# Optimization experiments

Measured on AMD Instinct MI355X. Metric: run time of the kernel, lower is better.

The kernel has to match this reference:

```python
import jax, jax.numpy as jnp
import numpy as np

LAMBDA = 25.0
MU = 25.0
NU = 1.0
ALPHA = 0.25
EPS = 1e-4
NUM_MATCHES = (20, 4)


def _cdist(a, b):
    # a: (B, Na, D), b: (B, Nb, D) -> euclidean distances (B, Na, Nb)
    d2 = (jnp.sum(a * a, axis=-1)[:, :, None]
          + jnp.sum(b * b, axis=-1)[:, None, :]
          - 2.0 * jnp.einsum('bnd,bmd->bnm', a, b))
    return jnp.sqrt(jnp.maximum(d2, 0.0))


def _nearest_neighbors(input_maps, candidate_maps, distances, num_matches):
    # Faithful to lightly.models.utils.nearest_neighbors:
    #  1) for each input element find its nearest candidate (argmin over last dim)
    #  2) keep the num_matches input elements with smallest nn distance
    # Indices are non-differentiable in torch, so stop_gradient on distances.
    distances = jax.lax.stop_gradient(distances)
    nn_idx = jnp.argmin(distances, axis=-1)           # (B, Na)
    nn_val = jnp.min(distances, axis=-1)              # (B, Na)
    _, min_idx = jax.lax.top_k(-nn_val, num_matches)  # smallest num_matches -> (B, M)
    filt_in = jnp.take_along_axis(input_maps, min_idx[..., None], axis=1)      # (B, M, C)
    cand_nn = jnp.take_along_axis(candidate_maps, nn_idx[..., None], axis=1)   # (B, Na, C)
    filt_cand = jnp.take_along_axis(cand_nn, min_idx[..., None], axis=1)       # (B, M, C)
    return filt_in, filt_cand


def _mse(a, b):
    return jnp.mean((a - b) ** 2)


def _variance_loss(x):
    # torch.var default is unbiased (ddof=1)
    std = jnp.sqrt(jnp.var(x, axis=0, ddof=1) + EPS)
    return jnp.mean(jax.nn.relu(1.0 - std))


def _covariance_loss(x):
    n, d = x.shape
    x = x - jnp.mean(x, axis=0)
    cov = (x.T @ x) / (n - 1)                         # (D, D)
    off = cov - jnp.diag(jnp.diag(cov))
    return jnp.sum(off ** 2) / d


def _global_loss(z_a, z_b):
    inv = _mse(z_a, z_b)
    var = 0.5 * (_variance_loss(z_a) + _variance_loss(z_b))
    cov = _covariance_loss(z_a) + _covariance_loss(z_b)
    return LAMBDA * inv + MU * var + NU * cov


def _local_loss(za, zb, ga, gb):
    B = za.shape[0]
    za = za.reshape(B, -1, za.shape[-1])              # (B, H*W, C)
    zb = zb.reshape(B, -1, zb.shape[-1])
    ga = ga.reshape(B, -1, 2)                          # (B, H*W, 2)
    gb = gb.reshape(B, -1, 2)
    has_local_view = za.shape[1] != zb.shape[1]
    nm = NUM_MATCHES[1] if has_local_view else NUM_MATCHES[0]
    # L2 feature-space matching
    fa, na = _nearest_neighbors(za, zb, _cdist(za, zb), nm)
    fb, nb = _nearest_neighbors(zb, za, _cdist(zb, za), nm)
    inv = 0.5 * _mse(fa, na) + 0.5 * _mse(fb, nb)
    # Grid (spatial) matching
    fa, na = _nearest_neighbors(za, zb, _cdist(ga, gb), NUM_MATCHES[0])
    fb, nb = _nearest_neighbors(zb, za, _cdist(gb, ga), NUM_MATCHES[1])
    inv = inv + 0.5 * _mse(fa, na) + 0.5 * _mse(fb, nb)
    return LAMBDA * inv


def setup_inputs() -> dict:
    key = jax.random.key(0)
    k1, k2, k3, k4, k5, k6 = jax.random.split(key, 6)
    B, D = 128, 8192
    H = W = 7
    return {
        'z_a': jax.random.normal(k1, (B, D), dtype=jnp.float32),
        'z_b': jax.random.normal(k2, (B, D), dtype=jnp.float32),
        'z_a_local_features': jax.random.normal(k3, (B, H, W, D), dtype=jnp.float32),
        'z_b_local_features': jax.random.normal(k4, (B, H, W, D), dtype=jnp.float32),
        'grid_a': jax.random.uniform(k5, (B, H, W, 2), dtype=jnp.float32),
        'grid_b': jax.random.uniform(k6, (B, H, W, 2), dtype=jnp.float32),
    }


def reference(z_a, z_b, z_a_local_features, z_b_local_features, grid_a, grid_b):
    g = _global_loss(z_a, z_b)
    l = _local_loss(z_a_local_features, z_b_local_features, grid_a, grid_b)
    return ALPHA * g + (1.0 - ALPHA) * l
```

## Files before the change

### kernel.cpp

```cpp
#include <hip/hip_runtime.h>
#include <math.h>

#define BATCH 128
#define DIM   8192
#define HW    49
#define PAIRS 2401
#define SLOT  2512

#define WS_MSE    0
#define WS_VARA   1
#define WS_VARB   2
#define WS_DIAGA  3
#define WS_DIAGB  4
#define WS_S1     5
#define WS_S2     6
#define WS_S3     7
#define WS_S4     8
#define WS_SK2A   9
#define WS_SK2B   10
#define COLS_OFF    16
#define GRAMA_OFF   32784
#define GRAMB_OFF   49168
#define GK2PART_OFF 65552
#define L1PART_BIG  2162704
#define WS_NEED_FLOATS (L1PART_BIG + 256 * SLOT)
#define L1PART_SMALL 65552

typedef __attribute__((ext_vector_type(8))) short bf16x8;
typedef __attribute__((ext_vector_type(4))) float f32x4;

__device__ __forceinline__ unsigned cvtpk(float lo, float hi) {
    unsigned r;
    asm("v_cvt_pk_bf16_f32 %0, %1, %2" : "=v"(r) : "v"(lo), "v"(hi));
    return r;
}
__device__ __forceinline__ bf16x8 cvt8(f32x4 a, f32x4 b) {
    union { unsigned u[4]; bf16x8 v; } r;
    r.u[0] = cvtpk(a.x, a.y); r.u[1] = cvtpk(a.z, a.w);
    r.u[2] = cvtpk(b.x, b.y); r.u[3] = cvtpk(b.z, b.w);
    return r.v;
}
__device__ __forceinline__ f32x4 ld4(const unsigned char* p) {
    return *(const f32x4*)p;
}
__device__ __forceinline__ void gload16(const float* g, unsigned char* l) {
    __builtin_amdgcn_global_load_lds(
        (const __attribute__((address_space(1))) void*)g,
        (__attribute__((address_space(3))) void*)l, 16, 0, 0);
}

template<bool RED>
__global__ __launch_bounds__(512) void uber(const float* __restrict__ za_l,
                                            const float* __restrict__ zb_l,
                                            const float* __restrict__ z_a,
                                            const float* __restrict__ z_b,
                                            float* __restrict__ ws,
                                            float* __restrict__ l1part)
{
    __shared__ __align__(16) unsigned char shm[100352];
    const int tid = threadIdx.x;

    if (blockIdx.x < 256) {
        unsigned char* buf0 = shm;
        unsigned char* buf1 = shm + 50176;
        const int wv = tid >> 6, lane = tid & 63;
        const int fr = lane & 15, kg = lane >> 4;
        const int batch = blockIdx.x >> 1;
        const int kh    = blockIdx.x & 1;
        const float* Az = za_l + (size_t)batch * HW * DIM + (size_t)kh * 4096;
        const float* Bz = zb_l + (size_t)batch * HW * DIM + (size_t)kh * 4096;

        const float* gp[7];
        int jb[7];
        const int half = lane >> 5, l5 = lane & 31;
#pragma unroll
        for (int i = 0; i < 7; ++i) {
            int j = wv + 8 * i;
            gp[i] = Az; jb[i] = -1;
            if (j < 49) {
                int row = 2 * j + half;
                const float* rbase = (row < 49) ? (Az + (size_t)row * DIM)
                                                : (Bz + (size_t)(row - 49) * DIM);
                gp[i] = rbase + ((l5 ^ (row & 31)) << 2);
                jb[i] = j << 10;
            }
        }

        const int wr = wv >> 2, wc = wv & 3;
        int ar0 = wr * 32 + fr;
        int ar1 = ar0 + 16; if (ar1 > 48) ar1 = 48;
        int bc  = wc * 16 + fr; if (bc > 48) bc = 48;
        const int brow = 49 + bc;
        const int aw0 = ar0 << 9, pa0 = ar0 & 31;
        const int aw1 = ar1 << 9, pa1 = ar1 & 31;
        const int bw  = brow << 9, pb = brow & 31;

        f32x4 acc00 = {0.f,0.f,0.f,0.f}, acc10 = {0.f,0.f,0.f,0.f};
        f32x4 aa0 = {0.f,0.f,0.f,0.f}, aa1 = {0.f,0.f,0.f,0.f}, bb = {0.f,0.f,0.f,0.f};

#define L1_ISSUE(DST, s) do {                                                  \
    _Pragma("unroll") for (int i = 0; i < 7; ++i)                              \
        if (jb[i] >= 0) gload16(gp[i] + (size_t)(s) * 128, (DST) + jb[i]);     \
    } while (0)

        L1_ISSUE(buf0, 0);
        __syncthreads();

        int p = 0;
#pragma unroll 1
        for (int s = 0; s < 32; ++s) {
            unsigned char* cur = p ? buf1 : buf0;
            unsigned char* nxt = p ? buf0 : buf1;
            if (s < 31) {
                L1_ISSUE(nxt, s + 1);
                __builtin_amdgcn_sched_barrier(0);
            }
#pragma unroll
            for (int kk = 0; kk < 4; ++kk) {
                const int s0 = kk * 8 + kg * 2;
                bf16x8 a0 = cvt8(ld4(cur + aw0 + (((s0)     ^ pa0) << 4)),
                                 ld4(cur + aw0 + (((s0 + 1) ^ pa0) << 4)));
                bf16x8 a1 = cvt8(ld4(cur + aw1 + (((s0)     ^ pa1) << 4)),
                                 ld4(cur + aw1 + (((s0 + 1) ^ pa1) << 4)));
                bf16x8 b0 = cvt8(ld4(cur + bw  + (((s0)     ^ pb ) << 4)),
                                 ld4(cur + bw  + (((s0 + 1) ^ pb ) << 4)));
                acc00 = __builtin_amdgcn_mfma_f32_16x16x32_bf16(a0, b0, acc00, 0, 0, 0);
                acc10 = __builtin_amdgcn_mfma_f32_16x16x32_bf16(a1, b0, acc10, 0, 0, 0);
                aa0   = __builtin_amdgcn_mfma_f32_16x16x32_bf16(a0, a0, aa0,   0, 0, 0);
                aa1   = __builtin_amdgcn_mfma_f32_16x16x32_bf16(a1, a1, aa1,   0, 0, 0);
                bb    = __builtin_amdgcn_mfma_f32_16x16x32_bf16(b0, b0, bb,    0, 0, 0);
            }
            __syncthreads();
            p ^= 1;
        }
#undef L1_ISSUE

        float* gout = l1part + (size_t)(RED ? blockIdx.x : batch) * SLOT;
        const int gc = wc * 16 + fr;
#pragma unroll
        for (int rr = 0; rr < 4; ++rr) {
            int gr0 = wr * 32 + kg * 4 + rr;
            int gr1 = gr0 + 16;
            if (gc < HW) {
                if (gr0 < HW) {
                    if (RED) gout[gr0 * HW + gc] = acc00[rr];
                    else atomicAdd(&gout[gr0 * HW + gc], acc00[rr]);
                }
                if (gr1 < HW) {
                    if (RED) gout[gr1 * HW + gc] = acc10[rr];
                    else atomicAdd(&gout[gr1 * HW + gc], acc10[rr]);
                }
            }
        }
        if (wc == 0) {
#pragma unroll
            for (int rr = 0; rr < 4; ++rr) {
                int i = kg * 4 + rr;
                if (i == fr) {
                    int r0 = wr * 32 + i;
                    if (RED) gout[PAIRS + r0] = aa0[rr];
                    else atomicAdd(&gout[PAIRS + r0], aa0[rr]);
                    int r1 = r0 + 16;
                    if (r1 < HW) {
                        if (RED) gout[PAIRS + r1] = aa1[rr];
                        else atomicAdd(&gout[PAIRS + r1], aa1[rr]);
                    }
                }
            }
        }
        if (wr == 0) {
#pragma unroll
            for (int rr = 0; rr < 4; ++rr) {
                int i = kg * 4 + rr;
                if (i == fr) {
                    int rb_ = wc * 16 + i;
                    if (rb_ < HW) {
                        if (RED) gout[PAIRS + HW + rb_] = bb[rr];
                        else atomicAdd(&gout[PAIRS + HW + rb_], bb[rr]);
                    }
                }
            }
        }
    } else {
        const int chunk = blockIdx.x - 256;
        float* sxA = (float*)shm;
        float* sxB = sxA + 128 * 68;
        float* scr = sxB + 128 * 68;
        const int ty = tid >> 5, tx = tid & 31;
        const int q = tid >> 6, cc = tid & 63;

        float accA[8][4], accB[8][4];
#pragma unroll
        for (int r = 0; r < 8; ++r)
#pragma unroll
            for (int c = 0; c < 4; ++c) { accA[r][c] = 0.f; accB[r][c] = 0.f; }
        float cSA[2] = {0.f,0.f}, cQA[2] = {0.f,0.f};
        float cSB[2] = {0.f,0.f}, cQB[2] = {0.f,0.f};
        float mse = 0.f;

#pragma unroll
        for (int st = 0; st < 2; ++st) {
            __syncthreads();
            for (int f = tid; f < 2048; f += 512) {
                int row = f >> 4, c4 = f & 15;
                const float4 a4 = *(const float4*)(z_a + (size_t)row * DIM + chunk * 128 + st * 64 + c4 * 4);
                const float4 b4 = *(const float4*)(z_b + (size_t)row * DIM + chunk * 128 + st * 64 + c4 * 4);
                *(float4*)(sxA + row * 68 + c4 * 4) = a4;
                *(float4*)(sxB + row * 68 + c4 * 4) = b4;
                float dx = a4.x - b4.x, dy = a4.y - b4.y, dz = a4.z - b4.z, dw = a4.w - b4.w;
                mse += dx * dx + dy * dy + dz * dz + dw * dw;
            }
            __syncthreads();
            for (int r = 0; r < 16; ++r) {
                float vA = sxA[(q * 16 + r) * 68 + cc];
                float vB = sxB[(q * 16 + r) * 68 + cc];
                cSA[st] += vA; cQA[st] += vA * vA;
                cSB[st] += vB; cQB[st] += vB * vB;
            }
            for (int k = 0; k < 64; k += 4) {
                float4 ar4[8], br4[8];
#pragma unroll
                for (int r = 0; r < 8; ++r) {
                    ar4[r] = *(const float4*)(sxA + (ty + 16 * r) * 68 + k);
                    br4[r] = *(const float4*)(sxB + (ty + 16 * r) * 68 + k);
                }
#pragma unroll
                for (int c = 0; c < 4; ++c) {
                    float4 ac4 = *(const float4*)(sxA + (tx + 32 * c) * 68 + k);
                    float4 bc4 = *(const float4*)(sxB + (tx + 32 * c) * 68 + k);
#pragma unroll
                    for (int r = 0; r < 8; ++r) {
                        accA[r][c] += ar4[r].x * ac4.x + ar4[r].y * ac4.y + ar4[r].z * ac4.z + ar4[r].w * ac4.w;
                        accB[r][c] += br4[r].x * bc4.x + br4[r].y * bc4.y + br4[r].z * bc4.z + br4[r].w * bc4.w;
                    }
                }
            }
        }
#pragma unroll
        for (int tens = 0; tens < 2; ++tens) {
            __syncthreads();
            scr[q * 64 + cc]        = tens ? cSB[0] : cSA[0];
            scr[512 + q * 64 + cc]  = tens ? cSB[1] : cSA[1];
            scr[1024 + q * 64 + cc] = tens ? cQB[0] : cQA[0];
            scr[1536 + q * 64 + cc] = tens ? cQB[1] : cQA[1];
            __syncthreads();
            if (tid < 128) {
                int st = tid >> 6, c2 = tid & 63;
                float s = 0.f, qq = 0.f;
#pragma unroll
                for (int g = 0; g < 8; ++g) {
                    s  += scr[st * 512 + g * 64 + c2];
                    qq += scr[1024 + st * 512 + g * 64 + c2];
                }
                int col = chunk * 128 + st * 64 + c2;
                float* C = ws + COLS_OFF + tens * 2 * DIM;
                C[col] = s; C[DIM + col] = qq;
            }
        }
        for (int o = 32; o; o >>= 1) mse += __shfl_xor(mse, o);
        if ((tid & 63) == 0) atomicAdd(&ws[WS_MSE], mse);
        if (RED) {
            float* P = ws + GK2PART_OFF + (size_t)chunk * 32768;
#pragma unroll
            for (int r = 0; r < 8; ++r)
#pragma unroll
                for (int c = 0; c < 4; ++c) {
                    P[(ty + 16 * r) * 128 + tx + 32 * c] = accA[r][c];
                    P[16384 + (ty + 16 * r) * 128 + tx + 32 * c] = accB[r][c];
                }
        } else {
#pragma unroll
            for (int r = 0; r < 8; ++r)
#pragma unroll
                for (int c = 0; c < 4; ++c) {
                    atomicAdd(&ws[GRAMA_OFF + (ty + 16 * r) * 128 + tx + 32 * c], accA[r][c]);
                    atomicAdd(&ws[GRAMB_OFF + (ty + 16 * r) * 128 + tx + 32 * c], accB[r][c]);
                }
        }
    }
}

template<bool RED>
__global__ __launch_bounds__(256) void merge2(const float* __restrict__ ga,
                                              const float* __restrict__ gb,
                                              float* __restrict__ ws,
                                              const float* __restrict__ l1part)
{
    __shared__ float d2f[PAIRS];
    __shared__ float d2g[PAIRS];
    __shared__ float nAs[49], nBs[49];
    __shared__ float gax[49], gay[49], gbx[49], gby[49];
    __shared__ float mval[4][49];
    __shared__ int   midx[4][49];

    const int b = blockIdx.x;
    const int tid = threadIdx.x;

    if (b < 128) {
        if (!RED) return;
        int gid = b * 256 + tid;
        int tensor = gid >> 14, e = gid & 16383;
        const float* P = ws + GK2PART_OFF + (size_t)tensor * 16384;
        float s = 0.f;
        for (int c = 0; c < 64; ++c) s += P[(size_t)c * 32768 + e];
        ws[(tensor ? GRAMB_OFF : GRAMA_OFF) + e] = s;
        return;
    }
    if (b < 160) {
        int col = (b - 128) * 256 + tid;
        float sa = ws[COLS_OFF + col];
        float qa = ws[COLS_OFF + DIM + col];
        float sb = ws[COLS_OFF + 2 * DIM + col];
        float qb = ws[COLS_OFF + 3 * DIM + col];
        float sA = qa - sa * sa * (1.0f / BATCH);
        float sB = qb - sb * sb * (1.0f / BATCH);
        float rA = fmaxf(0.f, 1.f - sqrtf(sA * (1.0f / (BATCH - 1)) + 1e-4f));
        float rB = fmaxf(0.f, 1.f - sqrtf(sB * (1.0f / (BATCH - 1)) + 1e-4f));
        float dA = sA * sA, dB = sB * sB;
        for (int o = 32; o; o >>= 1) {
            rA += __shfl_xor(rA, o);
            rB += __shfl_xor(rB, o);
            dA += __shfl_xor(dA, o);
            dB += __shfl_xor(dB, o);
        }
        if ((tid & 63) == 0) {
            atomicAdd(&ws[WS_VARA],  rA);
            atomicAdd(&ws[WS_VARB],  rB);
            atomicAdd(&ws[WS_DIAGA], dA);
            atomicAdd(&ws[WS_DIAGB], dB);
        }
        return;
    }

    const int batch = b - 160;
    const float* P0 = l1part + (size_t)batch * (RED ? (2 * SLOT) : SLOT);
    auto rd = [&](int off) -> float {
        if (!RED) return P0[off];
        return P0[off] + P0[SLOT + off];
    };

    if (tid < 49) nAs[tid] = rd(PAIRS + tid);
    else if (tid >= 64 && tid < 113) nBs[tid - 64] = rd(PAIRS + 49 + (tid - 64));
    if (tid >= 128 && tid < 177) {
        int i = tid - 128;
        gax[i] = ga[batch * 98 + i * 2];
        gay[i] = ga[batch * 98 + i * 2 + 1];
    } else if (tid >= 192 && tid < 241) {
        int i = tid - 192;
        gbx[i] = gb[batch * 98 + i * 2];
        gby[i] = gb[batch * 98 + i * 2 + 1];
    }
    __syncthreads();
    for (int e = tid; e < PAIRS; e += 256) {
        int i = e / 49, j = e - i * 49;
        d2f[e] = nAs[i] + nBs[j] - 2.0f * rd(e);
        float dx = gax[i] - gbx[j], dy = gay[i] - gby[j];
        d2g[e] = dx * dx + dy * dy;
    }
    __syncthreads();
    const int task = tid >> 6, l = tid & 63;
    if (l < 49) {
        float bv = 3.0e38f; int bi = 0;
        if (task == 0) {
            for (int j = 0; j < 49; ++j) { float v = d2f[l * 49 + j]; if (v < bv) { bv = v; bi = j; } }
        } else if (task == 1) {
            for (int i = 0; i < 49; ++i) { float v = d2f[i * 49 + l]; if (v < bv) { bv = v; bi = i; } }
        } else if (task == 2) {
            for (int j = 0; j < 49; ++j) { float v = d2g[l * 49 + j]; if (v < bv) { bv = v; bi = j; } }
        } else {
            for (int i = 0; i < 49; ++i) { float v = d2g[i * 49 + l]; if (v < bv) { bv = v; bi = i; } }
        }
        mval[task][l] = bv; midx[task][l] = bi;
    }
    __syncthreads();
    if (l < 49) {
        float v = mval[task][l];
        int rank = 0;
        for (int k = 0; k < 49; ++k) {
            float u = mval[task][k];
            rank += (u < v) || (u == v && k < l);
        }
        if (task == 0)      { if (rank < 20) atomicAdd(&ws[WS_S1], v); }
        else if (task == 1) { if (rank < 20) atomicAdd(&ws[WS_S2], v); }
        else if (task == 2) { if (rank < 20) atomicAdd(&ws[WS_S3], d2f[l * 49 + midx[2][l]]); }
        else                { if (rank < 4)  atomicAdd(&ws[WS_S4], d2f[midx[3][l] * 49 + l]); }
    }
}

__global__ __launch_bounds__(256) void gk3_cov(float* __restrict__ ws)
{
    __shared__ float r[128];
    __shared__ float sS;
    __shared__ float wrd[4];
    const int tid = threadIdx.x;
    const float* G = ws + (blockIdx.x ? GRAMB_OFF : GRAMA_OFF);
    if (tid < 128) {
        float s0 = 0.f, s1 = 0.f, s2 = 0.f, s3 = 0.f;
        for (int k = 0; k < 128; k += 4) {
            s0 += G[(k + 0) * 128 + tid];
            s1 += G[(k + 1) * 128 + tid];
            s2 += G[(k + 2) * 128 + tid];
            s3 += G[(k + 3) * 128 + tid];
        }
        r[tid] = (s0 + s1) + (s2 + s3);
    }
    __syncthreads();
    if (tid < 64) {
        float t = r[tid] + r[tid + 64];
        for (int o = 32; o; o >>= 1) t += __shfl_xor(t, o);
        if (tid == 0) sS = t;
    }
    __syncthreads();
    const float S = sS;
    float sk = 0.f;
    for (int e = tid; e < 16384; e += 256) {
        float K = G[e] - (r[e >> 7] + r[e & 127]) * (1.0f / 128.0f) + S * (1.0f / 16384.0f);
        sk += K * K;
    }
    for (int o = 32; o; o >>= 1) sk += __shfl_xor(sk, o);
    if ((tid & 63) == 0) wrd[tid >> 6] = sk;
    __syncthreads();
    if (tid == 0)
        ws[blockIdx.x ? WS_SK2B : WS_SK2A] = wrd[0] + wrd[1] + wrd[2] + wrd[3];
}

__global__ void gk4_final(const float* __restrict__ ws, float* __restrict__ out)
{
    if (threadIdx.x == 0) {
        float inv_g = ws[WS_MSE] * (1.0f / ((float)BATCH * (float)DIM));
        float varl  = 0.5f * (ws[WS_VARA] + ws[WS_VARB]) * (1.0f / (float)DIM);
        float cov   = (ws[WS_SK2A] - ws[WS_DIAGA] + ws[WS_SK2B] - ws[WS_DIAGB])
                      * (1.0f / (127.0f * 127.0f * (float)DIM));
        float gl = 25.0f * inv_g + 25.0f * varl + cov;
        float m20 = (float)BATCH * 20.0f * (float)DIM;
        float m4  = (float)BATCH * 4.0f  * (float)DIM;
        float invl = 0.5f * (ws[WS_S1] + ws[WS_S2] + ws[WS_S3]) / m20
                   + 0.5f * ws[WS_S4] / m4;
        out[0] = 0.25f * gl + 0.75f * (25.0f * invl);
    }
}

extern "C" void kernel_launch(void* const* d_in, const int* in_sizes, int n_in,
                              void* d_out, int out_size, void* d_ws, size_t ws_size,
                              hipStream_t stream)
{
    (void)in_sizes; (void)n_in; (void)out_size;
    const float* z_a = (const float*)d_in[0];
    const float* z_b = (const float*)d_in[1];
    const float* zla = (const float*)d_in[2];
    const float* zlb = (const float*)d_in[3];
    const float* ga  = (const float*)d_in[4];
    const float* gb  = (const float*)d_in[5];
    float* ws  = (float*)d_ws;
    float* out = (float*)d_out;

    const bool big = ws_size >= (size_t)WS_NEED_FLOATS * sizeof(float);

    if (big) {
        hipMemsetAsync(d_ws, 0, 16 * sizeof(float), stream);
        uber<true><<<320, 512, 0, stream>>>(zla, zlb, z_a, z_b, ws, ws + L1PART_BIG);
        merge2<true><<<288, 256, 0, stream>>>(ga, gb, ws, ws + L1PART_BIG);
        gk3_cov<<<2, 256, 0, stream>>>(ws);
        gk4_final<<<1, 64, 0, stream>>>(ws, out);
    } else {
        hipMemsetAsync(d_ws, 0, (size_t)(L1PART_SMALL + BATCH * SLOT) * sizeof(float), stream);
        uber<false><<<320, 512, 0, stream>>>(zla, zlb, z_a, z_b, ws, ws + L1PART_SMALL);
        merge2<false><<<288, 256, 0, stream>>>(ga, gb, ws, ws + L1PART_SMALL);
        gk3_cov<<<2, 256, 0, stream>>>(ws);
        gk4_final<<<1, 64, 0, stream>>>(ws, out);
    }
}
```

Before: 143.1 us.

## Triple-buffer local Gram loads with vmcnt waits and reorder block roles

Moves the local-feature Gram loop from double to triple buffering in LDS. It prefetches two stages ahead and uses explicit s_waitcnt vmcnt counts plus a raw s_barrier, replacing the two __syncthreads per iteration with one barrier. It also reorders the grid so the 64 global-loss blocks get the low block indices and are scheduled first. The cost is 150KB of LDS per block, which limits occupancy to one block per CU, and the hand-counted vmcnt values depend on how many loads each wave issues.

```diff
diff --git a/kernel.cpp b/kernel.cpp
--- a/kernel.cpp
+++ b/kernel.cpp
@@ -57,16 +57,18 @@
                                             float* __restrict__ ws,
                                             float* __restrict__ l1part)
 {
-    __shared__ __align__(16) unsigned char shm[100352];
+    __shared__ __align__(16) unsigned char shm[150528];
     const int tid = threadIdx.x;
 
-    if (blockIdx.x < 256) {
+    if (blockIdx.x >= 64) {
+        const int lb = blockIdx.x - 64;
         unsigned char* buf0 = shm;
         unsigned char* buf1 = shm + 50176;
+        unsigned char* buf2 = shm + 100352;
         const int wv = tid >> 6, lane = tid & 63;
         const int fr = lane & 15, kg = lane >> 4;
-        const int batch = blockIdx.x >> 1;
-        const int kh    = blockIdx.x & 1;
+        const int batch = lb >> 1;
+        const int kh    = lb & 1;
         const float* Az = za_l + (size_t)batch * HW * DIM + (size_t)kh * 4096;
         const float* Bz = zb_l + (size_t)batch * HW * DIM + (size_t)kh * 4096;
 
@@ -104,17 +106,24 @@
     } while (0)
 
         L1_ISSUE(buf0, 0);
-        __syncthreads();
-
-        int p = 0;
+        L1_ISSUE(buf1, 1);
+
+        int m = 0;
 #pragma unroll 1
         for (int s = 0; s < 32; ++s) {
-            unsigned char* cur = p ? buf1 : buf0;
-            unsigned char* nxt = p ? buf0 : buf1;
-            if (s < 31) {
-                L1_ISSUE(nxt, s + 1);
+            if (s == 31)      asm volatile("s_waitcnt vmcnt(0)" ::: "memory");
+            else if (wv == 0) asm volatile("s_waitcnt vmcnt(7)" ::: "memory");
+            else              asm volatile("s_waitcnt vmcnt(6)" ::: "memory");
+            __builtin_amdgcn_sched_barrier(0);
+            __builtin_amdgcn_s_barrier();
+            __builtin_amdgcn_sched_barrier(0);
+            if (s <= 29) {
+                int m2 = m + 2; if (m2 >= 3) m2 -= 3;
+                unsigned char* nxt = (m2 == 0) ? buf0 : (m2 == 1) ? buf1 : buf2;
+                L1_ISSUE(nxt, s + 2);
                 __builtin_amdgcn_sched_barrier(0);
             }
+            unsigned char* cur = (m == 0) ? buf0 : (m == 1) ? buf1 : buf2;
 #pragma unroll
             for (int kk = 0; kk < 4; ++kk) {
                 const int s0 = kk * 8 + kg * 2;
@@ -130,12 +139,11 @@
                 aa1   = __builtin_amdgcn_mfma_f32_16x16x32_bf16(a1, a1, aa1,   0, 0, 0);
                 bb    = __builtin_amdgcn_mfma_f32_16x16x32_bf16(b0, b0, bb,    0, 0, 0);
             }
-            __syncthreads();
-            p ^= 1;
+            m = (m == 2) ? 0 : m + 1;
         }
 #undef L1_ISSUE
 
-        float* gout = l1part + (size_t)(RED ? blockIdx.x : batch) * SLOT;
+        float* gout = l1part + (size_t)(RED ? lb : batch) * SLOT;
         const int gc = wc * 16 + fr;
 #pragma unroll
         for (int rr = 0; rr < 4; ++rr) {
@@ -182,7 +190,7 @@
             }
         }
     } else {
-        const int chunk = blockIdx.x - 256;
+        const int chunk = blockIdx.x;
         float* sxA = (float*)shm;
         float* sxB = sxA + 128 * 68;
         float* scr = sxB + 128 * 68;
```

Result: faster. 131.0 us (-8.4%).
